# Kernel optimization log

Measured on AMD Instinct MI355X. Metric: run time of the kernel, lower is better.

## Reference

```python
import jax, jax.numpy as jnp
import numpy as np

C = 0.01      # ball curvature
SC = 0.1      # sqrt(c)
K = 20        # neighbors
EPS = 1e-15


def _norm(v):
    return jnp.sqrt(jnp.clip(jnp.sum(v * v, -1, keepdims=True), EPS))


def expmap0(u):
    n = _norm(u)
    return jnp.tanh(SC * n) * u / (SC * n)


def logmap0(x):
    n = _norm(x)
    t = jnp.clip(SC * n, 0.0, 1.0 - 1e-7)
    return jnp.arctanh(t) * x / (SC * n)


def mobius_add(x, y):
    x2 = jnp.sum(x * x, -1, keepdims=True)
    y2 = jnp.sum(y * y, -1, keepdims=True)
    xy = jnp.sum(x * y, -1, keepdims=True)
    num = (1 + 2 * C * xy + C * y2) * x + (1 - C * x2) * y
    den = 1 + 2 * C * xy + C * C * x2 * y2
    return num / jnp.clip(den, EPS)


def knn(x, k):
    # x: (B,N,C) -> (B,N,k) indices of nearest neighbors (largest -dist^2)
    xx = jnp.sum(x * x, -1)                                 # (B,N)
    pd = 2.0 * jnp.einsum('bnc,bmc->bnm', x, x) - xx[:, :, None] - xx[:, None, :]
    return jax.lax.top_k(pd, k)[1]


def gather(x, idx):
    # x: (B,N,C), idx: (B,N,k) -> (B,N,k,C)
    return jax.vmap(lambda xt, ix: xt[ix])(x, idx)


def batchnorm(y, g, b, axes):
    mu = jnp.mean(y, axes)
    var = jnp.var(y, axes)
    return (y - mu) / jnp.sqrt(var + 1e-5) * g + b


def edge_block(x, w, g, b):
    # x: (B,N,C) -> (B,N,Cout); 1x1 conv over concat(nbr - ctr, ctr)
    idx = knn(x, K)
    nb = gather(x, idx)                                     # (B,N,K,C)
    ctr = jnp.broadcast_to(x[:, :, None, :], nb.shape)
    f = jnp.concatenate([nb - ctr, ctr], -1)                # (B,N,K,2C)
    y = jnp.einsum('bnkc,oc->bnko', f, w)
    y = jax.nn.leaky_relu(batchnorm(y, g, b, (0, 1, 2)), 0.2)
    return jnp.max(y, axis=2)


def setup_inputs():
    key = jax.random.key(0)
    ks = jax.random.split(key, 6)
    B, N = 8, 1024
    return {
        'x': jax.random.normal(ks[0], (B, 3, N), jnp.float32),
        'W1': jax.random.normal(ks[1], (64, 6), jnp.float32) * 0.1,
        'w2': jax.random.normal(ks[2], (64, 128), jnp.float32) * 0.05,
        'g2': jnp.ones((64,), jnp.float32), 'b2': jnp.zeros((64,), jnp.float32),
        'w3': jax.random.normal(ks[3], (128, 128), jnp.float32) * 0.05,
        'g3': jnp.ones((128,), jnp.float32), 'b3': jnp.zeros((128,), jnp.float32),
        'w4': jax.random.normal(ks[4], (256, 256), jnp.float32) * 0.05,
        'g4': jnp.ones((256,), jnp.float32), 'b4': jnp.zeros((256,), jnp.float32),
        'w5': jax.random.normal(ks[5], (1024, 512), jnp.float32) * 0.05,
        'g5': jnp.ones((1024,), jnp.float32), 'b5': jnp.zeros((1024,), jnp.float32),
    }


def reference(x, W1, w2, g2, b2, w3, g3, b3, w4, g4, b4, w5, g5, b5):
    xt = jnp.transpose(x, (0, 2, 1))                        # (B,N,3)
    # --- hyperbolic edge features ---
    idx = knn(xt, K)                                        # knn in euclidean coords
    xp = expmap0(xt)                                        # ToPoincare
    nb = gather(xp, idx)                                    # (B,N,K,3)
    ctr = jnp.broadcast_to(xp[:, :, None, :], nb.shape)
    h = jnp.concatenate([mobius_add(nb, -ctr), ctr], -1)    # (B,N,K,6)
    # MobiusConv2d (kernel 1) == mobius matvec: expmap0(W @ logmap0(x))
    h = expmap0(logmap0(h) @ W1.T)                          # (B,N,K,64)
    # MobiusBatchNorm2d (tangent-space normalization, bias=False)
    u = logmap0(h)
    mu = jnp.mean(u, axis=(0, 1, 2))
    uc = u - mu
    var = jnp.mean(jnp.sum(uc * uc, -1))
    h = expmap0(uc / jnp.sqrt(var + 1e-5))
    # Radial LeakyReLU in tangent space
    h = expmap0(jax.nn.leaky_relu(logmap0(h), 0.2))
    x1 = logmap0(jnp.max(h, axis=2))                        # max over k, FromPoincare -> (B,N,64)
    # --- euclidean DGCNN stack ---
    x2 = edge_block(x1, w2, g2, b2)                         # (B,N,64)
    x3 = edge_block(x2, w3, g3, b3)                         # (B,N,128)
    x4 = edge_block(x3, w4, g4, b4)                         # (B,N,256)
    feat = jnp.concatenate([x1, x2, x3, x4], -1)            # (B,N,512)
    y = jnp.einsum('bnc,oc->bno', feat, w5)                 # (B,N,1024)
    y = jax.nn.leaky_relu(batchnorm(y, g5, b5, (0, 1)), 0.2)
    return jnp.max(y, axis=1)                               # (B,1024)
```

## Files before the change

kernel.cpp:

```cpp
#include <hip/hip_runtime.h>
#include <math.h>

#define KNN 20
constexpr int B_ = 8, N_ = 1024, BN_ = B_ * N_;
constexpr int NEDGE = BN_ * KNN;

using f32x4 = __attribute__((ext_vector_type(4))) float;
using s8v = __attribute__((ext_vector_type(8))) short;
typedef unsigned long long u64;

__device__ __forceinline__ float wave_sum(float v) {
#pragma unroll
  for (int off = 32; off >= 1; off >>= 1) v += __shfl_xor(v, off, 64);
  return v;
}

__device__ __forceinline__ unsigned sortable(float f) {
  unsigned u = __float_as_uint(f);
  return u ^ ((u & 0x80000000u) ? 0xFFFFFFFFu : 0x80000000u);
}

__device__ __forceinline__ unsigned short rne_bf16(float f) {
  unsigned u = __float_as_uint(f);
  unsigned r = (u + 0x7FFFu + ((u >> 16) & 1u)) >> 16;
  return (unsigned short)r;
}

__device__ __forceinline__ u64 packkey(float v, int m) {
  return ((u64)sortable(v) << 10) | (u64)(1023 - m);
}

__device__ __forceinline__ void sort16_desc(u64 (&v)[16]) {
#pragma unroll
  for (int p = 1; p < 16; p <<= 1)
#pragma unroll
    for (int k = p; k >= 1; k >>= 1)
#pragma unroll
      for (int j = k & (p - 1); j + k < 16; j += 2 * k)
#pragma unroll
        for (int i = 0; i < k && i + j + k < 16; ++i)
          if ((i + j) / (2 * p) == (i + j + k) / (2 * p)) {
            u64 a = v[i + j], b = v[i + j + k];
            bool sw = a < b;
            v[i + j] = sw ? b : a;
            v[i + j + k] = sw ? a : b;
          }
}

__device__ __forceinline__ u64 bitonic64_desc(u64 B, int lane) {
#pragma unroll
  for (int k = 2; k <= 64; k <<= 1)
#pragma unroll
    for (int j = k >> 1; j > 0; j >>= 1) {
      u64 o = __shfl_xor(B, j, 64);
      bool up = ((lane & k) != 0);
      bool lower = ((lane & j) == 0);
      bool keepMin = (up == lower);
      bool takeOther = keepMin ? (o < B) : (o > B);
      B = takeOther ? o : B;
    }
  return B;
}

__device__ __forceinline__ void topk20_sorted(u64 (&v)[16], int lane,
                                              int* __restrict__ outp) {
  sort16_desc(v);
  u64 B = v[0];
#pragma unroll
  for (int s = 0; s < 15; ++s) v[s] = v[s + 1];
  v[15] = 0;
  B = bitonic64_desc(B, lane);
  for (int sel = 0; sel < KNN; ++sel) {
    u64 win = __shfl(B, 0, 64);
    int m = 1023 - (int)(win & 1023ull);
    if (lane == 0) outp[sel] = m;
    int origin = m & 63;
    u64 ins = __shfl(v[0], origin, 64);
    bool isorig = (lane == origin);
#pragma unroll
    for (int s = 0; s < 15; ++s) v[s] = isorig ? v[s + 1] : v[s];
    v[15] = isorig ? 0 : v[15];
    u64 Bs = __shfl_down(B, 1, 64);
    if (lane == 63) Bs = 0;
    unsigned long long ball = __ballot(Bs > ins);
    int pos = __popcll(ball);
    u64 Bup = __shfl_up(Bs, 1, 64);
    B = (lane < pos) ? Bs : (lane == pos ? ins : Bup);
  }
}

__global__ void k_prep2(const float* __restrict__ x, float* __restrict__ xp,
                        const float* __restrict__ w5,
                        unsigned short* __restrict__ w5b) {
  int bid = blockIdx.x;
  if (bid < 32) {
    int i = bid * 256 + threadIdx.x;
    int b = i >> 10, n = i & 1023;
    float v0 = x[(b * 3 + 0) * N_ + n];
    float v1 = x[(b * 3 + 1) * N_ + n];
    float v2 = x[(b * 3 + 2) * N_ + n];
    float nsq = v0 * v0 + v1 * v1 + v2 * v2;
    float nn = sqrtf(fmaxf(nsq, 1e-15f));
    float s = tanhf(0.1f * nn) / (0.1f * nn);
    xp[i * 3 + 0] = s * v0; xp[i * 3 + 1] = s * v1; xp[i * 3 + 2] = s * v2;
  } else {
    int e = ((bid - 32) * 256 + threadIdx.x) * 4;
    float4 v = *(const float4*)(w5 + e);
    ushort4 o;
    o.x = rne_bf16(v.x); o.y = rne_bf16(v.y); o.z = rne_bf16(v.z); o.w = rne_bf16(v.w);
    *(ushort4*)(w5b + e) = o;
  }
}

__global__ __launch_bounds__(256) void k_knn3s(const float* __restrict__ x,
                                               int* __restrict__ idx) {
  __shared__ float4 pts4[N_];
  int t = threadIdx.x;
  int row0 = blockIdx.x * 4;
  int b = row0 >> 10;
  const float* xb = x + (size_t)b * 3 * N_;
  for (int i = t; i < N_; i += 256) {
    float px = xb[i], py = xb[N_ + i], pz = xb[2 * N_ + i];
    pts4[i] = make_float4(px, py, pz, px * px + py * py + pz * pz);
  }
  __syncthreads();
  int lane = t & 63, w = t >> 6;
  int row = row0 + w, rl = row & 1023;
  float4 c = pts4[rl];
  u64 v[16];
#pragma unroll
  for (int s = 0; s < 16; ++s) {
    int m = lane + 64 * s;
    float4 q = pts4[m];
    float dot = c.x * q.x + c.y * q.y + c.z * q.z;
    float val = 2.f * dot - c.w - q.w;
    v[s] = packkey(val, m);
  }
  topk20_sorted(v, lane, idx + (size_t)row * KNN);
}

__global__ __launch_bounds__(256) void k_topks(const float* __restrict__ pd,
                                               int* __restrict__ idx) {
  int t = threadIdx.x, lane = t & 63, w = t >> 6;
  int row = blockIdx.x * 4 + w;
  const float* rp = pd + (size_t)row * N_;
  u64 v[16];
#pragma unroll
  for (int s = 0; s < 16; ++s) v[s] = packkey(rp[lane + 64 * s], lane + 64 * s);
  topk20_sorted(v, lane, idx + (size_t)row * KNN);
}

__global__ __launch_bounds__(256) void k_hgeom(const float* __restrict__ xp,
                                               const int* __restrict__ idx,
                                               float* __restrict__ fgeo,
                                               float* __restrict__ mom) {
  int e = blockIdx.x * 256 + threadIdx.x;
  int gw = e / KNN;
  int b = gw >> 10;
  int nbr = idx[e];
  const float* pc = xp + (size_t)gw * 3;
  float c0 = pc[0], c1 = pc[1], c2 = pc[2];
  const float* pn = xp + ((size_t)(b << 10) + nbr) * 3;
  float a0 = pn[0], a1 = pn[1], a2 = pn[2];
  float x2 = a0 * a0 + a1 * a1 + a2 * a2;
  float y2 = c0 * c0 + c1 * c1 + c2 * c2;
  float xy = -(a0 * c0 + a1 * c1 + a2 * c2);
  float f1 = 1.f + 0.02f * xy + 0.01f * y2;
  float f2 = 1.f - 0.01f * x2;
  float den = 1.f + 0.02f * xy + 0.0001f * x2 * y2;
  float rden = 1.f / fmaxf(den, 1e-15f);
  float m0 = (f1 * a0 - f2 * c0) * rden;
  float m1 = (f1 * a1 - f2 * c1) * rden;
  float m2 = (f1 * a2 - f2 * c2) * rden;
  float nsq = m0 * m0 + m1 * m1 + m2 * m2 + y2;
  float nn = sqrtf(fmaxf(nsq, 1e-15f));
  float sn = 0.1f * nn;
  float tt = fminf(sn, 1.f - 1e-7f);
  float s = atanhf(tt) / sn;
  float f[6] = {s * m0, s * m1, s * m2, s * c0, s * c1, s * c2};
#pragma unroll
  for (int j = 0; j < 6; ++j) fgeo[j * NEDGE + e] = f[j];
  float mm[27];
  {
    int q = 0;
#pragma unroll
    for (int i = 0; i < 6; ++i) mm[q++] = f[i];
#pragma unroll
    for (int i = 0; i < 6; ++i)
#pragma unroll
      for (int j = i; j < 6; ++j) mm[q++] = f[i] * f[j];
  }
#pragma unroll
  for (int m = 0; m < 27; ++m) mm[m] = wave_sum(mm[m]);
  __shared__ float part[4][27];
  int lane = threadIdx.x & 63, w = threadIdx.x >> 6;
  if (lane == 0) {
#pragma unroll
    for (int m = 0; m < 27; ++m) part[w][m] = mm[m];
  }
  __syncthreads();
  int t = threadIdx.x;
  if (t < 27) {
    float v = part[0][t] + part[1][t] + part[2][t] + part[3][t];
    atomicAdd(&mom[t * 16 + (blockIdx.x & 15)], v);
  }
}

__global__ void k_hfin2(const float* __restrict__ mom,
                        const float* __restrict__ w1, float* mu64,
                        float* invv) {
  __shared__ float M[27];
  int t = threadIdx.x;
  if (t < 27) {
    float s = 0.f;
    for (int k = 0; k < 16; ++k) s += mom[t * 16 + k];
    M[t] = s * (1.f / (float)NEDGE);
  }
  __syncthreads();
  float w1r[6];
#pragma unroll
  for (int j = 0; j < 6; ++j) w1r[j] = w1[t * 6 + j];
  float mu = 0.f;
#pragma unroll
  for (int j = 0; j < 6; ++j) mu = fmaf(w1r[j], M[j], mu);
  float q = 0.f;
  {
    int off = 6;
#pragma unroll
    for (int i = 0; i < 6; ++i) {
      q = fmaf(w1r[i] * w1r[i], M[off], q); ++off;
#pragma unroll
      for (int j = i + 1; j < 6; ++j) {
        q = fmaf(2.f * w1r[i] * w1r[j], M[off], q); ++off;
      }
    }
  }
  float varc = q - mu * mu;
  float var = wave_sum(varc);
  mu64[t] = mu;
  if (t == 0) invv[0] = 1.f / sqrtf(var + 1e-5f);
}

__global__ __launch_bounds__(256) void k_hyper_x1(
    const float* __restrict__ fgeo, const float* __restrict__ w1,
    const float* __restrict__ mu64, const float* __restrict__ invv,
    float* __restrict__ x1, float* __restrict__ xx,
    unsigned short* __restrict__ fb) {
  int t = threadIdx.x, lane = t & 63, w = t >> 6;
  int gw = blockIdx.x * 4 + w;
  float w1r[6];
#pragma unroll
  for (int j = 0; j < 6; ++j) w1r[j] = w1[lane * 6 + j];
  float f[6] = {0.f, 0.f, 0.f, 0.f, 0.f, 0.f};
  if (lane < KNN) {
    int e = gw * KNN + lane;
#pragma unroll
    for (int j = 0; j < 6; ++j) f[j] = fgeo[j * NEDGE + e];
  }
  float mu = mu64[lane];
  float inv = invv[0];
  float mx = -INFINITY;
  for (int k = 0; k < KNN; ++k) {
    float u = 0.f;
#pragma unroll
    for (int j = 0; j < 6; ++j) u = fmaf(w1r[j], __shfl(f[j], k), u);
    float vv = (u - mu) * inv;
    float l = vv > 0.f ? vv : 0.2f * vv;
    float nsq = wave_sum(l * l);
    float nn = sqrtf(fmaxf(nsq, 1e-15f));
    float sn = 0.1f * nn;
    float sc = tanhf(sn) / sn;
    mx = fmaxf(mx, sc * l);
  }
  float msq = wave_sum(mx * mx);
  float mn = sqrtf(fmaxf(msq, 1e-15f));
  float sn = 0.1f * mn;
  float tt = fminf(sn, 1.f - 1e-7f);
  float val = atanhf(tt) / sn * mx;
  x1[(size_t)gw * 64 + lane] = val;
  fb[(size_t)gw * 512 + lane] = rne_bf16(val);
  float xs = wave_sum(val * val);
  if (lane == 0) xx[gw] = xs;
}

__device__ __forceinline__ void load_t68(float (&Lt)[64][68],
                                         const float* __restrict__ src,
                                         int ldr, int t) {
  int row = t >> 2, kq = (t & 3) * 16;
  const float* p = src + (size_t)row * ldr + kq;
  float4 v0 = *(const float4*)(p);
  float4 v1 = *(const float4*)(p + 4);
  float4 v2 = *(const float4*)(p + 8);
  float4 v3 = *(const float4*)(p + 12);
  Lt[kq + 0][row] = v0.x;  Lt[kq + 1][row] = v0.y;
  Lt[kq + 2][row] = v0.z;  Lt[kq + 3][row] = v0.w;
  Lt[kq + 4][row] = v1.x;  Lt[kq + 5][row] = v1.y;
  Lt[kq + 6][row] = v1.z;  Lt[kq + 7][row] = v1.w;
  Lt[kq + 8][row] = v2.x;  Lt[kq + 9][row] = v2.y;
  Lt[kq + 10][row] = v2.z; Lt[kq + 11][row] = v2.w;
  Lt[kq + 12][row] = v3.x; Lt[kq + 13][row] = v3.y;
  Lt[kq + 14][row] = v3.z; Lt[kq + 15][row] = v3.w;
}

template <int CIN>
__global__ __launch_bounds__(256) void k_pdsym(const float* __restrict__ xin,
                                               const float* __restrict__ xx,
                                               float* __restrict__ pd) {
  __shared__ float At[64][68], Bt[64][68];
  int b = blockIdx.z;
  int id = blockIdx.x;
  int i = 0, rem = id;
  while (rem >= 16 - i) { rem -= 16 - i; ++i; }
  int j = i + rem;
  int n0 = i << 6, m0 = j << 6;
  int t = threadIdx.x;
  int tr4 = (t >> 4) * 4, tc4 = (t & 15) * 4;
  float acc[4][4] = {};
  const float* xb = xin + (size_t)b * N_ * CIN;
  for (int c0 = 0; c0 < CIN; c0 += 64) {
    if (c0) __syncthreads();
    load_t68(At, xb + (size_t)n0 * CIN + c0, CIN, t);
    load_t68(Bt, xb + (size_t)m0 * CIN + c0, CIN, t);
    __syncthreads();
#pragma unroll 4
    for (int k = 0; k < 64; ++k) {
      float4 a = *(const float4*)&At[k][tr4];
      float4 bb = *(const float4*)&Bt[k][tc4];
      float av[4] = {a.x, a.y, a.z, a.w};
      float bv[4] = {bb.x, bb.y, bb.z, bb.w};
#pragma unroll
      for (int ii = 0; ii < 4; ++ii)
#pragma unroll
        for (int jj = 0; jj < 4; ++jj) acc[ii][jj] = fmaf(av[ii], bv[jj], acc[ii][jj]);
    }
  }
  const float* xxn = xx + b * N_;
  float v[4][4];
#pragma unroll
  for (int ii = 0; ii < 4; ++ii) {
    int r = n0 + tr4 + ii;
#pragma unroll
    for (int jj = 0; jj < 4; ++jj) {
      int c = m0 + tc4 + jj;
      v[ii][jj] = 2.f * acc[ii][jj] - xxn[r] - xxn[c];
      pd[((size_t)b * N_ + r) * N_ + c] = v[ii][jj];
    }
  }
  if (i != j) {
    __syncthreads();
#pragma unroll
    for (int ii = 0; ii < 4; ++ii)
#pragma unroll
      for (int jj = 0; jj < 4; ++jj) At[tc4 + jj][tr4 + ii] = v[ii][jj];
    __syncthreads();
#pragma unroll
    for (int ii = 0; ii < 4; ++ii) {
      float4 rv = *(const float4*)&At[tr4 + ii][tc4];
      *(float4*)&pd[((size_t)b * N_ + m0 + tr4 + ii) * N_ + n0 + tc4] = rv;
    }
  }
}

template <int CIN, int COUT>
__global__ __launch_bounds__(256) void k_xw2(const float* __restrict__ xin,
                                             const float* __restrict__ w,
                                             float* __restrict__ Y,
                                             float* __restrict__ Z) {
  __shared__ float At[64][68], Bt[64][68];
  int n0 = blockIdx.x * 64;
  int j0 = blockIdx.y * 64;
  float* outp; int obase, coff;
  if (j0 < COUT) { outp = Y; obase = j0; coff = 0; }
  else { outp = Z; obase = j0 - COUT; coff = CIN; }
  int t = threadIdx.x;
  int tr4 = (t >> 4) * 4, tc4 = (t & 15) * 4;
  float acc[4][4] = {};
  for (int c0 = 0; c0 < CIN; c0 += 64) {
    if (c0) __syncthreads();
    load_t68(At, xin + (size_t)n0 * CIN + c0, CIN, t);
    load_t68(Bt, w + (size_t)obase * (2 * CIN) + coff + c0, 2 * CIN, t);
    __syncthreads();
#pragma unroll 4
    for (int k = 0; k < 64; ++k) {
      float4 a = *(const float4*)&At[k][tr4];
      float4 bb = *(const float4*)&Bt[k][tc4];
      float av[4] = {a.x, a.y, a.z, a.w};
      float bv[4] = {bb.x, bb.y, bb.z, bb.w};
#pragma unroll
      for (int ii = 0; ii < 4; ++ii)
#pragma unroll
        for (int jj = 0; jj < 4; ++jj) acc[ii][jj] = fmaf(av[ii], bv[jj], acc[ii][jj]);
    }
  }
#pragma unroll
  for (int ii = 0; ii < 4; ++ii)
#pragma unroll
    for (int jj = 0; jj < 4; ++jj)
      outp[(size_t)(n0 + tr4 + ii) * COUT + obase + tc4 + jj] = acc[ii][jj];
}

template <int COUT>
__global__ __launch_bounds__(256) void k_gather2(
    const float* __restrict__ Y, const float* __restrict__ Z,
    const int* __restrict__ idx, float* gsum, float* gsq,
    float* __restrict__ xout) {
  constexpr int J = COUT / 64;
  int t = threadIdx.x, lane = t & 63, w = t >> 6;
  int bn = blockIdx.x * 4 + w;
  int b = bn >> 10;
  int myidx = 0;
  if (lane < KNN) myidx = idx[(size_t)bn * KNN + lane];
  float base[J], acc[J], acc2[J], mx[J];
#pragma unroll
  for (int j = 0; j < J; ++j) {
    int o = lane + 64 * j;
    base[j] = Z[(size_t)bn * COUT + o] - Y[(size_t)bn * COUT + o];
    acc[j] = 0.f; acc2[j] = 0.f; mx[j] = -INFINITY;
  }
  for (int k = 0; k < KNN; ++k) {
    int nbr = __shfl(myidx, k);
    const float* yr = Y + ((size_t)(b << 10) + nbr) * COUT;
#pragma unroll
    for (int j = 0; j < J; ++j) {
      float v = yr[lane + 64 * j] + base[j];
      acc[j] += v; acc2[j] += v * v; mx[j] = fmaxf(mx[j], v);
    }
  }
  int bkt = bn & 31;
#pragma unroll
  for (int j = 0; j < J; ++j) {
    atomicAdd(&gsum[bkt * 1024 + lane + 64 * j], acc[j]);
    atomicAdd(&gsq[bkt * 1024 + lane + 64 * j], acc2[j]);
    xout[(size_t)bn * COUT + lane + 64 * j] = mx[j];
  }
}

template <int COUT, bool WXX, bool WOUT>
__global__ void k_apply(float* __restrict__ xio,
                        const float* __restrict__ aArr,
                        const float* __restrict__ cArr,
                        unsigned short* __restrict__ fb, int coloff,
                        float* __restrict__ xx) {
  constexpr int J = COUT / 64;
  int t = threadIdx.x, lane = t & 63, w = t >> 6;
  int bn = blockIdx.x * 4 + w;
  float s = 0.f;
#pragma unroll
  for (int j = 0; j < J; ++j) {
    int o = lane + 64 * j;
    float v = xio[(size_t)bn * COUT + o];
    float u = aArr[o] * v + cArr[o];
    u = u > 0.f ? u : 0.2f * u;
    if (WOUT) xio[(size_t)bn * COUT + o] = u;
    fb[(size_t)bn * 512 + coloff + o] = rne_bf16(u);
    if (WXX) s = fmaf(u, u, s);
  }
  if (WXX) {
    s = wave_sum(s);
    if (lane == 0) xx[bn] = s;
  }
}

__global__ void k_bnfin(const float* gsum, const float* gsq,
                        const float* __restrict__ g, const float* __restrict__ bb,
                        float* aArr, float* cArr, int COUT, float Minv) {
  int ch = blockIdx.x * 256 + threadIdx.x;
  if (ch >= COUT) return;
  float S = 0, S2 = 0;
  for (int k = 0; k < 32; ++k) { S += gsum[k * 1024 + ch]; S2 += gsq[k * 1024 + ch]; }
  float mu = S * Minv;
  float var = S2 * Minv - mu * mu;
  float a = g[ch] / sqrtf(var + 1e-5f);
  aArr[ch] = a;
  cArr[ch] = bb[ch] - mu * a;
}

__global__ __launch_bounds__(256) void k_fgemm3(
    const unsigned short* __restrict__ fb, const unsigned short* __restrict__ wb,
    float* gsum, float* gsq, float* __restrict__ pmax) {
  __shared__ unsigned short Bs[64][264];
  int t = threadIdx.x, lane = t & 63, w = t >> 6;
  int m0 = blockIdx.x * 128;
  int j0 = blockIdx.y * 64;
  int r16 = lane & 15, kg = lane >> 4;
  f32x4 acc[2][4];
#pragma unroll
  for (int mi = 0; mi < 2; ++mi)
#pragma unroll
    for (int nj = 0; nj < 4; ++nj) acc[mi][nj] = {0.f, 0.f, 0.f, 0.f};
  const unsigned short* pa0 = fb + (size_t)(m0 + w * 32 + r16) * 512 + kg * 8;
  const unsigned short* pa1 = pa0 + 16 * 512;
  s8v a0 = *(const s8v*)pa0;
  s8v a1 = *(const s8v*)pa1;
  int kglob = 0;
  for (int kh = 0; kh < 2; ++kh) {
    if (kh) __syncthreads();
#pragma unroll
    for (int it = 0; it < 8; ++it) {
      int chunk = it * 256 + t;
      int row = chunk >> 5;
      int kc = (chunk & 31) * 8;
      *(s8v*)&Bs[row][kc] =
          *(const s8v*)(wb + (size_t)(j0 + row) * 512 + kh * 256 + kc);
    }
    __syncthreads();
#pragma unroll
    for (int ki = 0; ki < 8; ++ki) {
      s8v na0 = a0, na1 = a1;
      int knext = kglob + 32;
      if (knext < 512) {
        na0 = *(const s8v*)(pa0 + knext);
        na1 = *(const s8v*)(pa1 + knext);
      }
      int kl = ki * 32 + kg * 8;
      s8v b0 = *(const s8v*)&Bs[r16][kl];
      s8v b1 = *(const s8v*)&Bs[r16 + 16][kl];
      s8v b2 = *(const s8v*)&Bs[r16 + 32][kl];
      s8v b3 = *(const s8v*)&Bs[r16 + 48][kl];
      acc[0][0] = __builtin_amdgcn_mfma_f32_16x16x32_bf16(a0, b0, acc[0][0], 0, 0, 0);
      acc[0][1] = __builtin_amdgcn_mfma_f32_16x16x32_bf16(a0, b1, acc[0][1], 0, 0, 0);
      acc[0][2] = __builtin_amdgcn_mfma_f32_16x16x32_bf16(a0, b2, acc[0][2], 0, 0, 0);
      acc[0][3] = __builtin_amdgcn_mfma_f32_16x16x32_bf16(a0, b3, acc[0][3], 0, 0, 0);
      acc[1][0] = __builtin_amdgcn_mfma_f32_16x16x32_bf16(a1, b0, acc[1][0], 0, 0, 0);
      acc[1][1] = __builtin_amdgcn_mfma_f32_16x16x32_bf16(a1, b1, acc[1][1], 0, 0, 0);
      acc[1][2] = __builtin_amdgcn_mfma_f32_16x16x32_bf16(a1, b2, acc[1][2], 0, 0, 0);
      acc[1][3] = __builtin_amdgcn_mfma_f32_16x16x32_bf16(a1, b3, acc[1][3], 0, 0, 0);
      a0 = na0; a1 = na1; kglob = knext;
    }
  }
  float s[4], s2[4], mx[4];
#pragma unroll
  for (int nj = 0; nj < 4; ++nj) {
    s[nj] = 0.f; s2[nj] = 0.f; mx[nj] = -INFINITY;
#pragma unroll
    for (int mi = 0; mi < 2; ++mi)
#pragma unroll
      for (int r = 0; r < 4; ++r) {
        float v = acc[mi][nj][r];
        s[nj] += v; s2[nj] += v * v; mx[nj] = fmaxf(mx[nj], v);
      }
    s[nj] += __shfl_xor(s[nj], 16, 64);  s[nj] += __shfl_xor(s[nj], 32, 64);
    s2[nj] += __shfl_xor(s2[nj], 16, 64); s2[nj] += __shfl_xor(s2[nj], 32, 64);
    mx[nj] = fmaxf(mx[nj], __shfl_xor(mx[nj], 16, 64));
    mx[nj] = fmaxf(mx[nj], __shfl_xor(mx[nj], 32, 64));
  }
  __shared__ float wsum[4][64], wsq[4][64], wmax[4][64];
  if (lane < 16) {
#pragma unroll
    for (int nj = 0; nj < 4; ++nj) {
      wsum[w][nj * 16 + lane] = s[nj];
      wsq[w][nj * 16 + lane] = s2[nj];
      wmax[w][nj * 16 + lane] = mx[nj];
    }
  }
  __syncthreads();
  if (t < 64) {
    float S = 0.f, S2 = 0.f, MX = -INFINITY;
#pragma unroll
    for (int ww = 0; ww < 4; ++ww) {
      S += wsum[ww][t]; S2 += wsq[ww][t]; MX = fmaxf(MX, wmax[ww][t]);
    }
    int o = j0 + t;
    int bkt = blockIdx.x & 31;
    atomicAdd(&gsum[bkt * 1024 + o], S);
    atomicAdd(&gsq[bkt * 1024 + o], S2);
    pmax[(size_t)(blockIdx.x & 7) * 8192 + (blockIdx.x >> 3) * 1024 + o] = MX;
  }
}

__global__ void k_fmax2(const float* __restrict__ pmax,
                        const float* __restrict__ aArr,
                        const float* __restrict__ cArr, float* __restrict__ out) {
  int j = blockIdx.x * 256 + threadIdx.x;
  int o = j & 1023;
  float mx = -INFINITY;
#pragma unroll
  for (int c = 0; c < 8; ++c) mx = fmaxf(mx, pmax[c * 8192 + j]);
  float v = aArr[o] * mx + cArr[o];
  v = v > 0.f ? v : 0.2f * v;
  out[j] = v;
}

extern "C" void kernel_launch(void* const* d_in, const int* in_sizes, int n_in,
                              void* d_out, int out_size, void* d_ws,
                              size_t ws_size, hipStream_t stream) {
  const float* x  = (const float*)d_in[0];
  const float* w1 = (const float*)d_in[1];
  const float* w2 = (const float*)d_in[2];
  const float* g2 = (const float*)d_in[3];
  const float* b2 = (const float*)d_in[4];
  const float* w3 = (const float*)d_in[5];
  const float* g3 = (const float*)d_in[6];
  const float* b3 = (const float*)d_in[7];
  const float* w4 = (const float*)d_in[8];
  const float* g4 = (const float*)d_in[9];
  const float* b4 = (const float*)d_in[10];
  const float* w5 = (const float*)d_in[11];
  const float* g5 = (const float*)d_in[12];
  const float* b5 = (const float*)d_in[13];

  float* W = (float*)d_ws;
  float* xp = W + 24576;
  float* xx = W + 49152;
  float* stats = W + 57344;
  float* aArr = stats + 262144;
  float* cArr = stats + 263168;
  float* mu64 = stats + 264192;
  float* invv = stats + 264256;
  float* mom  = stats + 264320;
  float* x1 = W + 323584;
  float* x2 = W + 847872;
  float* x3 = W + 1372160;
  float* x4 = W + 2420736;
  float* pd = W + 4517888;
  float* Y  = pd;
  float* Z  = pd + 2097152;
  float* fgeo = pd;
  int* idx = (int*)(W + 12906496);
  unsigned short* featb = (unsigned short*)(W + 13070336);
  unsigned short* w5b = (unsigned short*)(W + 13070336 + 2097152);
  float* pmax = x3;
  float* out = (float*)d_out;

  const float MinvE = 1.f / (float)(BN_ * KNN);
  float* gs0 = stats;           float* gq0 = stats + 32768;
  float* gs1 = stats + 65536;   float* gq1 = stats + 98304;
  float* gs2 = stats + 131072;  float* gq2 = stats + 163840;
  float* gs3 = stats + 196608;  float* gq3 = stats + 229376;

  hipMemsetAsync(stats, 0, 264832 * sizeof(float), stream);

  k_prep2<<<32 + 512, 256, 0, stream>>>(x, xp, w5, w5b);
  k_knn3s<<<2048, 256, 0, stream>>>(x, idx);
  k_hgeom<<<640, 256, 0, stream>>>(xp, idx, fgeo, mom);
  k_hfin2<<<1, 64, 0, stream>>>(mom, w1, mu64, invv);
  k_hyper_x1<<<2048, 256, 0, stream>>>(fgeo, w1, mu64, invv, x1, xx, featb);

  k_pdsym<64><<<dim3(136, 1, 8), 256, 0, stream>>>(x1, xx, pd);
  k_topks<<<2048, 256, 0, stream>>>(pd, idx);
  k_xw2<64, 64><<<dim3(128, 2), 256, 0, stream>>>(x1, w2, Y, Z);
  k_gather2<64><<<2048, 256, 0, stream>>>(Y, Z, idx, gs0, gq0, x2);
  k_bnfin<<<1, 256, 0, stream>>>(gs0, gq0, g2, b2, aArr, cArr, 64, MinvE);
  k_apply<64, true, true><<<2048, 256, 0, stream>>>(x2, aArr, cArr, featb, 64, xx);

  k_pdsym<64><<<dim3(136, 1, 8), 256, 0, stream>>>(x2, xx, pd);
  k_topks<<<2048, 256, 0, stream>>>(pd, idx);
  k_xw2<64, 128><<<dim3(128, 4), 256, 0, stream>>>(x2, w3, Y, Z);
  k_gather2<128><<<2048, 256, 0, stream>>>(Y, Z, idx, gs1, gq1, x3);
  k_bnfin<<<1, 256, 0, stream>>>(gs1, gq1, g3, b3, aArr, cArr, 128, MinvE);
  k_apply<128, true, true><<<2048, 256, 0, stream>>>(x3, aArr, cArr, featb, 128, xx);

  k_pdsym<128><<<dim3(136, 1, 8), 256, 0, stream>>>(x3, xx, pd);
  k_topks<<<2048, 256, 0, stream>>>(pd, idx);
  k_xw2<128, 256><<<dim3(128, 8), 256, 0, stream>>>(x3, w4, Y, Z);
  k_gather2<256><<<2048, 256, 0, stream>>>(Y, Z, idx, gs2, gq2, x4);
  k_bnfin<<<1, 256, 0, stream>>>(gs2, gq2, g4, b4, aArr, cArr, 256, MinvE);
  k_apply<256, false, false><<<2048, 256, 0, stream>>>(x4, aArr, cArr, featb, 256, xx);

  k_fgemm3<<<dim3(64, 16), 256, 0, stream>>>(featb, w5b, gs3, gq3, pmax);
  k_bnfin<<<4, 256, 0, stream>>>(gs3, gq3, g5, b5, aArr, cArr, 1024, 1.f / (float)BN_);
  k_fmax2<<<32, 256, 0, stream>>>(pmax, aArr, cArr, out);
}
```

Before: 427.7 us.

## Fuse small launches: merge knn into prep, pd with xw, bnfin into fmax

Merges the first kNN kernel into the prep kernel, folds the hyperbolic batchnorm finalize into each k_hyper_x1 block, and combines the pairwise-distance and feature-transform GEMMs of edge blocks 1 and 2 into one launch by partitioning the grid. For those two blocks Y/Z move to the x4 buffer so they no longer overlap pd. The final BN finalize moves into the max kernel, and the fgemm A-operand prefetch is deepened to two steps. Together these remove several kernel launches and dependency gaps, at the cost of redundant per-block statistic reduction and higher register pressure.

Result: faster. 413.5 us (-3.3%).

```diff
diff --git a/kernel.cpp b/kernel.cpp
--- a/kernel.cpp
+++ b/kernel.cpp
@@ -89,12 +89,38 @@
   }
 }
 
-__global__ void k_prep2(const float* __restrict__ x, float* __restrict__ xp,
-                        const float* __restrict__ w5,
-                        unsigned short* __restrict__ w5b) {
+__global__ __launch_bounds__(256) void k_prep3(const float* __restrict__ x,
+                                               float* __restrict__ xp,
+                                               const float* __restrict__ w5,
+                                               unsigned short* __restrict__ w5b,
+                                               int* __restrict__ idx) {
   int bid = blockIdx.x;
-  if (bid < 32) {
-    int i = bid * 256 + threadIdx.x;
+  int t = threadIdx.x;
+  if (bid < 2048) {
+    __shared__ float4 pts4[N_];
+    int row0 = bid * 4;
+    int b = row0 >> 10;
+    const float* xb = x + (size_t)b * 3 * N_;
+    for (int i = t; i < N_; i += 256) {
+      float px = xb[i], py = xb[N_ + i], pz = xb[2 * N_ + i];
+      pts4[i] = make_float4(px, py, pz, px * px + py * py + pz * pz);
+    }
+    __syncthreads();
+    int lane = t & 63, w = t >> 6;
+    int row = row0 + w, rl = row & 1023;
+    float4 c = pts4[rl];
+    u64 v[16];
+#pragma unroll
+    for (int s = 0; s < 16; ++s) {
+      int m = lane + 64 * s;
+      float4 q = pts4[m];
+      float dot = c.x * q.x + c.y * q.y + c.z * q.z;
+      float val = 2.f * dot - c.w - q.w;
+      v[s] = packkey(val, m);
+    }
+    topk20_sorted(v, lane, idx + (size_t)row * KNN);
+  } else if (bid < 2080) {
+    int i = (bid - 2048) * 256 + t;
     int b = i >> 10, n = i & 1023;
     float v0 = x[(b * 3 + 0) * N_ + n];
     float v1 = x[(b * 3 + 1) * N_ + n];
@@ -104,39 +130,12 @@
     float s = tanhf(0.1f * nn) / (0.1f * nn);
     xp[i * 3 + 0] = s * v0; xp[i * 3 + 1] = s * v1; xp[i * 3 + 2] = s * v2;
   } else {
-    int e = ((bid - 32) * 256 + threadIdx.x) * 4;
+    int e = ((bid - 2080) * 256 + t) * 4;
     float4 v = *(const float4*)(w5 + e);
     ushort4 o;
     o.x = rne_bf16(v.x); o.y = rne_bf16(v.y); o.z = rne_bf16(v.z); o.w = rne_bf16(v.w);
     *(ushort4*)(w5b + e) = o;
   }
-}
-
-__global__ __launch_bounds__(256) void k_knn3s(const float* __restrict__ x,
-                                               int* __restrict__ idx) {
-  __shared__ float4 pts4[N_];
-  int t = threadIdx.x;
-  int row0 = blockIdx.x * 4;
-  int b = row0 >> 10;
-  const float* xb = x + (size_t)b * 3 * N_;
-  for (int i = t; i < N_; i += 256) {
-    float px = xb[i], py = xb[N_ + i], pz = xb[2 * N_ + i];
-    pts4[i] = make_float4(px, py, pz, px * px + py * py + pz * pz);
-  }
-  __syncthreads();
-  int lane = t & 63, w = t >> 6;
-  int row = row0 + w, rl = row & 1023;
-  float4 c = pts4[rl];
-  u64 v[16];
-#pragma unroll
-  for (int s = 0; s < 16; ++s) {
-    int m = lane + 64 * s;
-    float4 q = pts4[m];
-    float dot = c.x * q.x + c.y * q.y + c.z * q.z;
-    float val = 2.f * dot - c.w - q.w;
-    v[s] = packkey(val, m);
-  }
-  topk20_sorted(v, lane, idx + (size_t)row * KNN);
 }
 
 __global__ __launch_bounds__(256) void k_topks(const float* __restrict__ pd,
@@ -206,47 +205,41 @@
   }
 }
 
-__global__ void k_hfin2(const float* __restrict__ mom,
-                        const float* __restrict__ w1, float* mu64,
-                        float* invv) {
-  __shared__ float M[27];
-  int t = threadIdx.x;
+__global__ __launch_bounds__(256) void k_hyper_x1(
+    const float* __restrict__ fgeo, const float* __restrict__ w1,
+    const float* __restrict__ mom, float* __restrict__ x1,
+    float* __restrict__ xx, unsigned short* __restrict__ fb) {
+  __shared__ float Msh[27], muS[64], invS;
+  int t = threadIdx.x, lane = t & 63, w = t >> 6;
   if (t < 27) {
     float s = 0.f;
     for (int k = 0; k < 16; ++k) s += mom[t * 16 + k];
-    M[t] = s * (1.f / (float)NEDGE);
+    Msh[t] = s * (1.f / (float)NEDGE);
   }
   __syncthreads();
-  float w1r[6];
-#pragma unroll
-  for (int j = 0; j < 6; ++j) w1r[j] = w1[t * 6 + j];
-  float mu = 0.f;
-#pragma unroll
-  for (int j = 0; j < 6; ++j) mu = fmaf(w1r[j], M[j], mu);
-  float q = 0.f;
-  {
+  if (t < 64) {
+    float w1r[6];
+#pragma unroll
+    for (int j = 0; j < 6; ++j) w1r[j] = w1[t * 6 + j];
+    float mu = 0.f;
+#pragma unroll
+    for (int j = 0; j < 6; ++j) mu = fmaf(w1r[j], Msh[j], mu);
+    float q = 0.f;
     int off = 6;
 #pragma unroll
     for (int i = 0; i < 6; ++i) {
-      q = fmaf(w1r[i] * w1r[i], M[off], q); ++off;
+      q = fmaf(w1r[i] * w1r[i], Msh[off], q); ++off;
 #pragma unroll
       for (int j = i + 1; j < 6; ++j) {
-        q = fmaf(2.f * w1r[i] * w1r[j], M[off], q); ++off;
+        q = fmaf(2.f * w1r[i] * w1r[j], Msh[off], q); ++off;
       }
     }
-  }
-  float varc = q - mu * mu;
-  float var = wave_sum(varc);
-  mu64[t] = mu;
-  if (t == 0) invv[0] = 1.f / sqrtf(var + 1e-5f);
-}
-
-__global__ __launch_bounds__(256) void k_hyper_x1(
-    const float* __restrict__ fgeo, const float* __restrict__ w1,
-    const float* __restrict__ mu64, const float* __restrict__ invv,
-    float* __restrict__ x1, float* __restrict__ xx,
-    unsigned short* __restrict__ fb) {
-  int t = threadIdx.x, lane = t & 63, w = t >> 6;
+    float varc = q - mu * mu;
+    float var = wave_sum(varc);
+    muS[t] = mu;
+    if (t == 0) invS = 1.f / sqrtf(var + 1e-5f);
+  }
+  __syncthreads();
   int gw = blockIdx.x * 4 + w;
   float w1r[6];
 #pragma unroll
@@ -257,8 +250,8 @@
 #pragma unroll
     for (int j = 0; j < 6; ++j) f[j] = fgeo[j * NEDGE + e];
   }
-  float mu = mu64[lane];
-  float inv = invv[0];
+  float mu = muS[lane];
+  float inv = invS;
   float mx = -INFINITY;
   for (int k = 0; k < KNN; ++k) {
     float u = 0.f;
@@ -303,17 +296,15 @@
 }
 
 template <int CIN>
-__global__ __launch_bounds__(256) void k_pdsym(const float* __restrict__ xin,
-                                               const float* __restrict__ xx,
-                                               float* __restrict__ pd) {
-  __shared__ float At[64][68], Bt[64][68];
-  int b = blockIdx.z;
-  int id = blockIdx.x;
-  int i = 0, rem = id;
+__device__ __forceinline__ void pd_body(const float* __restrict__ xin,
+                                        const float* __restrict__ xx,
+                                        float* __restrict__ pd, int b, int tri,
+                                        int t, float (&At)[64][68],
+                                        float (&Bt)[64][68]) {
+  int i = 0, rem = tri;
   while (rem >= 16 - i) { rem -= 16 - i; ++i; }
   int j = i + rem;
   int n0 = i << 6, m0 = j << 6;
-  int t = threadIdx.x;
   int tr4 = (t >> 4) * 4, tc4 = (t & 15) * 4;
   float acc[4][4] = {};
   const float* xb = xin + (size_t)b * N_ * CIN;
@@ -362,17 +353,17 @@
 }
 
 template <int CIN, int COUT>
-__global__ __launch_bounds__(256) void k_xw2(const float* __restrict__ xin,
-                                             const float* __restrict__ w,
-                                             float* __restrict__ Y,
-                                             float* __restrict__ Z) {
-  __shared__ float At[64][68], Bt[64][68];
-  int n0 = blockIdx.x * 64;
-  int j0 = blockIdx.y * 64;
+__device__ __forceinline__ void xw_body(const float* __restrict__ xin,
+                                        const float* __restrict__ w,
+                                        float* __restrict__ Y,
+                                        float* __restrict__ Z, int bid, int t,
+                                        float (&At)[64][68],
+                                        float (&Bt)[64][68]) {
+  int n0 = (bid & 127) * 64;
+  int j0 = (bid >> 7) * 64;
   float* outp; int obase, coff;
   if (j0 < COUT) { outp = Y; obase = j0; coff = 0; }
   else { outp = Z; obase = j0 - COUT; coff = CIN; }
-  int t = threadIdx.x;
   int tr4 = (t >> 4) * 4, tc4 = (t & 15) * 4;
   float acc[4][4] = {};
   for (int c0 = 0; c0 < CIN; c0 += 64) {
@@ -399,6 +390,42 @@
       outp[(size_t)(n0 + tr4 + ii) * COUT + obase + tc4 + jj] = acc[ii][jj];
 }
 
+template <int CIN, int COUT>
+__global__ __launch_bounds__(256) void k_pdxw(const float* __restrict__ xin,
+                                              const float* __restrict__ xx,
+                                              float* __restrict__ pd,
+                                              const float* __restrict__ w,
+                                              float* __restrict__ Y,
+                                              float* __restrict__ Z) {
+  __shared__ float At[64][68], Bt[64][68];
+  int id = blockIdx.x;
+  int t = threadIdx.x;
+  if (id < 1088) {
+    int b = id / 136, tri = id - b * 136;
+    pd_body<CIN>(xin, xx, pd, b, tri, t, At, Bt);
+  } else {
+    xw_body<CIN, COUT>(xin, w, Y, Z, id - 1088, t, At, Bt);
+  }
+}
+
+template <int CIN>
+__global__ __launch_bounds__(256) void k_pdsym(const float* __restrict__ xin,
+                                               const float* __restrict__ xx,
+                                               float* __restrict__ pd) {
+  __shared__ float At[64][68], Bt[64][68];
+  pd_body<CIN>(xin, xx, pd, blockIdx.z, blockIdx.x, threadIdx.x, At, Bt);
+}
+
+template <int CIN, int COUT>
+__global__ __launch_bounds__(256) void k_xw2(const float* __restrict__ xin,
+                                             const float* __restrict__ w,
+                                             float* __restrict__ Y,
+                                             float* __restrict__ Z) {
+  __shared__ float At[64][68], Bt[64][68];
+  int bid = blockIdx.x + blockIdx.y * 128;
+  xw_body<CIN, COUT>(xin, w, Y, Z, bid, threadIdx.x, At, Bt);
+}
+
 template <int COUT>
 __global__ __launch_bounds__(256) void k_gather2(
     const float* __restrict__ Y, const float* __restrict__ Z,
@@ -490,8 +517,8 @@
     for (int nj = 0; nj < 4; ++nj) acc[mi][nj] = {0.f, 0.f, 0.f, 0.f};
   const unsigned short* pa0 = fb + (size_t)(m0 + w * 32 + r16) * 512 + kg * 8;
   const unsigned short* pa1 = pa0 + 16 * 512;
-  s8v a0 = *(const s8v*)pa0;
-  s8v a1 = *(const s8v*)pa1;
+  s8v aC0 = *(const s8v*)pa0,        aC1 = *(const s8v*)pa1;
+  s8v aN0 = *(const s8v*)(pa0 + 32), aN1 = *(const s8v*)(pa1 + 32);
   int kglob = 0;
   for (int kh = 0; kh < 2; ++kh) {
     if (kh) __syncthreads();
@@ -506,26 +533,26 @@
     __syncthreads();
 #pragma unroll
     for (int ki = 0; ki < 8; ++ki) {
-      s8v na0 = a0, na1 = a1;
-      int knext = kglob + 32;
-      if (knext < 512) {
-        na0 = *(const s8v*)(pa0 + knext);
-        na1 = *(const s8v*)(pa1 + knext);
+      s8v aF0 = aN0, aF1 = aN1;
+      int kf = kglob + 64;
+      if (kf < 512) {
+        aF0 = *(const s8v*)(pa0 + kf);
+        aF1 = *(const s8v*)(pa1 + kf);
       }
       int kl = ki * 32 + kg * 8;
       s8v b0 = *(const s8v*)&Bs[r16][kl];
       s8v b1 = *(const s8v*)&Bs[r16 + 16][kl];
       s8v b2 = *(const s8v*)&Bs[r16 + 32][kl];
       s8v b3 = *(const s8v*)&Bs[r16 + 48][kl];
-      acc[0][0] = __builtin_amdgcn_mfma_f32_16x16x32_bf16(a0, b0, acc[0][0], 0, 0, 0);
-      acc[0][1] = __builtin_amdgcn_mfma_f32_16x16x32_bf16(a0, b1, acc[0][1], 0, 0, 0);
-      acc[0][2] = __builtin_amdgcn_mfma_f32_16x16x32_bf16(a0, b2, acc[0][2], 0, 0, 0);
-      acc[0][3] = __builtin_amdgcn_mfma_f32_16x16x32_bf16(a0, b3, acc[0][3], 0, 0, 0);
-      acc[1][0] = __builtin_amdgcn_mfma_f32_16x16x32_bf16(a1, b0, acc[1][0], 0, 0, 0);
-      acc[1][1] = __builtin_amdgcn_mfma_f32_16x16x32_bf16(a1, b1, acc[1][1], 0, 0, 0);
-      acc[1][2] = __builtin_amdgcn_mfma_f32_16x16x32_bf16(a1, b2, acc[1][2], 0, 0, 0);
-      acc[1][3] = __builtin_amdgcn_mfma_f32_16x16x32_bf16(a1, b3, acc[1][3], 0, 0, 0);
-      a0 = na0; a1 = na1; kglob = knext;
+      acc[0][0] = __builtin_amdgcn_mfma_f32_16x16x32_bf16(aC0, b0, acc[0][0], 0, 0, 0);
+      acc[0][1] = __builtin_amdgcn_mfma_f32_16x16x32_bf16(aC0, b1, acc[0][1], 0, 0, 0);
+      acc[0][2] = __builtin_amdgcn_mfma_f32_16x16x32_bf16(aC0, b2, acc[0][2], 0, 0, 0);
+      acc[0][3] = __builtin_amdgcn_mfma_f32_16x16x32_bf16(aC0, b3, acc[0][3], 0, 0, 0);
+      acc[1][0] = __builtin_amdgcn_mfma_f32_16x16x32_bf16(aC1, b0, acc[1][0], 0, 0, 0);
+      acc[1][1] = __builtin_amdgcn_mfma_f32_16x16x32_bf16(aC1, b1, acc[1][1], 0, 0, 0);
+      acc[1][2] = __builtin_amdgcn_mfma_f32_16x16x32_bf16(aC1, b2, acc[1][2], 0, 0, 0);
+      acc[1][3] = __builtin_amdgcn_mfma_f32_16x16x32_bf16(aC1, b3, acc[1][3], 0, 0, 0);
+      aC0 = aN0; aC1 = aN1; aN0 = aF0; aN1 = aF1; kglob += 32;
     }
   }
   float s[4], s2[4], mx[4];
@@ -568,15 +595,23 @@
   }
 }
 
-__global__ void k_fmax2(const float* __restrict__ pmax,
-                        const float* __restrict__ aArr,
-                        const float* __restrict__ cArr, float* __restrict__ out) {
+__global__ void k_fmax3(const float* __restrict__ pmax, const float* gsum,
+                        const float* gsq, const float* __restrict__ g,
+                        const float* __restrict__ bb, float* __restrict__ out) {
   int j = blockIdx.x * 256 + threadIdx.x;
   int o = j & 1023;
+  float S = 0.f, S2 = 0.f;
+#pragma unroll 8
+  for (int k = 0; k < 32; ++k) { S += gsum[k * 1024 + o]; S2 += gsq[k * 1024 + o]; }
+  const float Minv = 1.f / (float)BN_;
+  float mu = S * Minv;
+  float var = S2 * Minv - mu * mu;
+  float a = g[o] / sqrtf(var + 1e-5f);
+  float c = bb[o] - mu * a;
   float mx = -INFINITY;
 #pragma unroll
-  for (int c = 0; c < 8; ++c) mx = fmaxf(mx, pmax[c * 8192 + j]);
-  float v = aArr[o] * mx + cArr[o];
+  for (int ch = 0; ch < 8; ++ch) mx = fmaxf(mx, pmax[ch * 8192 + j]);
+  float v = a * mx + c;
   v = v > 0.f ? v : 0.2f * v;
   out[j] = v;
 }
@@ -605,16 +640,14 @@
   float* stats = W + 57344;
   float* aArr = stats + 262144;
   float* cArr = stats + 263168;
-  float* mu64 = stats + 264192;
-  float* invv = stats + 264256;
   float* mom  = stats + 264320;
   float* x1 = W + 323584;
   float* x2 = W + 847872;
   float* x3 = W + 1372160;
   float* x4 = W + 2420736;
   float* pd = W + 4517888;
-  float* Y  = pd;
-  float* Z  = pd + 2097152;
+  float* Y4 = pd;
+  float* Z4 = pd + 2097152;
   float* fgeo = pd;
   int* idx = (int*)(W + 12906496);
   unsigned short* featb = (unsigned short*)(W + 13070336);
@@ -622,6 +655,9 @@
   float* pmax = x3;
   float* out = (float*)d_out;
 
+  float* Y2 = x4;             float* Z2 = x4 + 524288;
+  float* Y3 = x4;             float* Z3 = x4 + 1048576;
+
   const float MinvE = 1.f / (float)(BN_ * KNN);
   float* gs0 = stats;           float* gq0 = stats + 32768;
   float* gs1 = stats + 65536;   float* gq1 = stats + 98304;
@@ -630,34 +666,29 @@
 
   hipMemsetAsync(stats, 0, 264832 * sizeof(float), stream);
 
-  k_prep2<<<32 + 512, 256, 0, stream>>>(x, xp, w5, w5b);
-  k_knn3s<<<2048, 256, 0, stream>>>(x, idx);
+  k_prep3<<<2592, 256, 0, stream>>>(x, xp, w5, w5b, idx);
   k_hgeom<<<640, 256, 0, stream>>>(xp, idx, fgeo, mom);
-  k_hfin2<<<1, 64, 0, stream>>>(mom, w1, mu64, invv);
-  k_hyper_x1<<<2048, 256, 0, stream>>>(fgeo, w1, mu64, invv, x1, xx, featb);
-
-  k_pdsym<64><<<dim3(136, 1, 8), 256, 0, stream>>>(x1, xx, pd);
+  k_hyper_x1<<<2048, 256, 0, stream>>>(fgeo, w1, mom, x1, xx, featb);
+
+  k_pdxw<64, 64><<<1088 + 256, 256, 0, stream>>>(x1, xx, pd, w2, Y2, Z2);
   k_topks<<<2048, 256, 0, stream>>>(pd, idx);
-  k_xw2<64, 64><<<dim3(128, 2), 256, 0, stream>>>(x1, w2, Y, Z);
-  k_gather2<64><<<2048, 256, 0, stream>>>(Y, Z, idx, gs0, gq0, x2);
+  k_gather2<64><<<2048, 256, 0, stream>>>(Y2, Z2, idx, gs0, gq0, x2);
   k_bnfin<<<1, 256, 0, stream>>>(gs0, gq0, g2, b2, aArr, cArr, 64, MinvE);
   k_apply<64, true, true><<<2048, 256, 0, stream>>>(x2, aArr, cArr, featb, 64, xx);
 
-  k_pdsym<64><<<dim3(136, 1, 8), 256, 0, stream>>>(x2, xx, pd);
+  k_pdxw<64, 128><<<1088 + 512, 256, 0, stream>>>(x2, xx, pd, w3, Y3, Z3);
   k_topks<<<2048, 256, 0, stream>>>(pd, idx);
-  k_xw2<64, 128><<<dim3(128, 4), 256, 0, stream>>>(x2, w3, Y, Z);
-  k_gather2<128><<<2048, 256, 0, stream>>>(Y, Z, idx, gs1, gq1, x3);
+  k_gather2<128><<<2048, 256, 0, stream>>>(Y3, Z3, idx, gs1, gq1, x3);
   k_bnfin<<<1, 256, 0, stream>>>(gs1, gq1, g3, b3, aArr, cArr, 128, MinvE);
   k_apply<128, true, true><<<2048, 256, 0, stream>>>(x3, aArr, cArr, featb, 128, xx);
 
   k_pdsym<128><<<dim3(136, 1, 8), 256, 0, stream>>>(x3, xx, pd);
   k_topks<<<2048, 256, 0, stream>>>(pd, idx);
-  k_xw2<128, 256><<<dim3(128, 8), 256, 0, stream>>>(x3, w4, Y, Z);
-  k_gather2<256><<<2048, 256, 0, stream>>>(Y, Z, idx, gs2, gq2, x4);
+  k_xw2<128, 256><<<dim3(128, 8), 256, 0, stream>>>(x3, w4, Y4, Z4);
+  k_gather2<256><<<2048, 256, 0, stream>>>(Y4, Z4, idx, gs2, gq2, x4);
   k_bnfin<<<1, 256, 0, stream>>>(gs2, gq2, g4, b4, aArr, cArr, 256, MinvE);
   k_apply<256, false, false><<<2048, 256, 0, stream>>>(x4, aArr, cArr, featb, 256, xx);
 
   k_fgemm3<<<dim3(64, 16), 256, 0, stream>>>(featb, w5b, gs3, gq3, pmax);
-  k_bnfin<<<4, 256, 0, stream>>>(gs3, gq3, g5, b5, aArr, cArr, 1024, 1.f / (float)BN_);
-  k_fmax2<<<32, 256, 0, stream>>>(pmax, aArr, cArr, out);
-}
+  k_fmax3<<<32, 256, 0, stream>>>(pmax, gs3, gq3, g5, b5, out);
+}
```
